# Kernel tuning notes

Measured on AMD Instinct MI355X. Metric: run time of the kernel, lower is better.

The kernel has to match this reference:

```python
import jax, jax.numpy as jnp
import numpy as np

B, S, D, H = 2, 2048, 1024, 16
DEPTH = D // H


def setup_inputs() -> dict:
    key = jax.random.key(0)
    ks = jax.random.split(key, 13)
    std = 1.0 / np.sqrt(D)
    inp = {
        'q': jax.random.normal(ks[0], (B, S, D), jnp.float32),
        'k': jax.random.normal(ks[1], (B, S, D), jnp.float32),
        'v': jax.random.normal(ks[2], (B, S, D), jnp.float32),
        # padding-style mask broadcastable to [B,H,Sq,Sk]; 1 = masked
        'mask': (jax.random.uniform(ks[3], (B, 1, 1, S)) < 0.1).astype(jnp.float32),
        'wq_w': jax.random.uniform(ks[4], (D, D), jnp.float32, -std, std),
        'wq_b': jax.random.uniform(ks[5], (D,), jnp.float32, -std, std),
        'wk_w': jax.random.uniform(ks[6], (D, D), jnp.float32, -std, std),
        'wk_b': jax.random.uniform(ks[7], (D,), jnp.float32, -std, std),
        'wv_w': jax.random.uniform(ks[8], (D, D), jnp.float32, -std, std),
        'wv_b': jax.random.uniform(ks[9], (D,), jnp.float32, -std, std),
        'wo_w': jax.random.uniform(ks[10], (D, D), jnp.float32, -std, std),
        'wo_b': jax.random.uniform(ks[11], (D,), jnp.float32, -std, std),
    }
    return inp


def _split_heads(x):
    # [B,S,D] -> [B,H,S,depth]
    b, s, _ = x.shape
    return x.reshape(b, s, H, DEPTH).transpose(0, 2, 1, 3)


def reference(q, k, v, mask, wq_w, wq_b, wk_w, wk_b, wv_w, wv_b, wo_w, wo_b):
    qh = _split_heads(q @ wq_w.T + wq_b)
    kh = _split_heads(k @ wk_w.T + wk_b)
    vh = _split_heads(v @ wv_w.T + wv_b)
    scale = 1.0 / jnp.sqrt(jnp.float32(DEPTH))
    logits = jnp.einsum('bhqd,bhkd->bhqk', qh, kh) * scale  # [B,H,S,S]
    logits = logits + mask * (-1e9)
    weights = jax.nn.softmax(logits, axis=-1)
    attn = jnp.einsum('bhqk,bhkd->bhqd', weights, vh)
    concat = attn.transpose(0, 2, 1, 3).reshape(q.shape[0], -1, D)
    out = concat @ wo_w.T + wo_b
    return out, weights
```

## Files before the change

### kernel.cpp

```cpp
#include <hip/hip_runtime.h>
#include <stdint.h>
#include <stddef.h>

static constexpr int NB = 2;
static constexpr int SS = 2048;
static constexpr int DDim = 1024;
static constexpr int NH = 16;
static constexpr size_t BSD = (size_t)NB * SS * DDim;
static constexpr size_t DDn = (size_t)DDim * DDim;

typedef __attribute__((ext_vector_type(4))) float f32x4;
typedef __attribute__((ext_vector_type(8))) short bf16x8;
typedef __attribute__((ext_vector_type(4))) short bf16x4;

static constexpr float SCL2 = 0.125f * 1.4426950408889634f;
static constexpr float MSK2 = -1.4426950408889634e9f;

__device__ __forceinline__ short f2bf(float f) {
  union { float f; unsigned u; } v; v.f = f;
  unsigned r = v.u + 0x7FFFu + ((v.u >> 16) & 1u);
  return (short)(r >> 16);
}

__device__ __forceinline__ void gload_lds16(const void* src, void* dst) {
  __builtin_amdgcn_global_load_lds(
      (const __attribute__((address_space(1))) void*)src,
      (__attribute__((address_space(3))) void*)dst, 16, 0, 0);
}

__global__ void cvt_all_k(const float* __restrict__ q, const float* __restrict__ k,
                          const float* __restrict__ v, const float* __restrict__ w0,
                          const float* __restrict__ w1, const float* __restrict__ w2,
                          const float* __restrict__ w3, short* __restrict__ out) {
  int i = blockIdx.x * 256 + threadIdx.x;
  const float* src;
  int j;
  if (i < 1572864) {
    int mat = i >> 19;
    src = mat == 0 ? q : mat == 1 ? k : v;
    j = i & 524287;
  } else {
    int t = i - 1572864;
    int mat = t >> 17;
    src = mat == 0 ? w0 : mat == 1 ? w1 : mat == 2 ? w2 : w3;
    j = t & 131071;
  }
  const f32x4* p = (const f32x4*)src + (size_t)j * 2;
  f32x4 a = p[0], c = p[1];
  bf16x8 o;
  o[0] = f2bf(a[0]); o[1] = f2bf(a[1]); o[2] = f2bf(a[2]); o[3] = f2bf(a[3]);
  o[4] = f2bf(c[0]); o[5] = f2bf(c[1]); o[6] = f2bf(c[2]); o[7] = f2bf(c[3]);
  ((bf16x8*)out)[i] = o;
}

__global__ __launch_bounds__(256, 2) void proj3_k(
    const short* __restrict__ Acat, const short* __restrict__ Bcat,
    const float* __restrict__ bq, const float* __restrict__ bk, const float* __restrict__ bv,
    short* __restrict__ qh, short* __restrict__ kh, short* __restrict__ vhT) {
  __shared__ short la[2][4096], lb[2][4096];
  const int tid = threadIdx.x, wid = tid >> 6, lane = tid & 63;
  const int proj = blockIdx.z;
  const short* A = Acat + (size_t)proj * BSD;
  const short* Bm = Bcat + (size_t)proj * DDn;
  const float* bias = proj == 0 ? bq : proj == 1 ? bk : bv;
  const int bM = blockIdx.y * 128, bN = blockIdx.x * 128;
  const int ar = lane & 15, ak = (lane >> 4) * 8;
  const int srow = lane >> 2, scol = (lane & 3) * 8;
  const int wr = wid >> 1, wc = wid & 1;
  f32x4 acc[4][4];
#pragma unroll
  for (int m = 0; m < 4; ++m)
#pragma unroll
    for (int n = 0; n < 4; ++n) acc[m][n] = (f32x4){0.f, 0.f, 0.f, 0.f};

  auto stage = [&](int kt, int bb) {
    const int k0 = kt * 32;
#pragma unroll
    for (int c = 0; c < 2; ++c) {
      int chunk = c * 4 + wid;
      gload_lds16(A + (size_t)(bM + chunk * 16 + srow) * DDim + k0 + scol, &la[bb][chunk * 512]);
      gload_lds16(Bm + (size_t)(bN + chunk * 16 + srow) * DDim + k0 + scol, &lb[bb][chunk * 512]);
    }
  };

  stage(0, 0);
  asm volatile("s_waitcnt vmcnt(0)" ::: "memory");
  __syncthreads();
  for (int kt = 0; kt < 32; ++kt) {
    const int bb = kt & 1;
    if (kt < 31) stage(kt + 1, bb ^ 1);
    bf16x8 af[4], bfr[4];
#pragma unroll
    for (int m = 0; m < 4; ++m)
      af[m] = *(const bf16x8*)(&la[bb][(wr * 64 + m * 16 + ar) * 32 + ak]);
#pragma unroll
    for (int n = 0; n < 4; ++n)
      bfr[n] = *(const bf16x8*)(&lb[bb][(wc * 64 + n * 16 + ar) * 32 + ak]);
#pragma unroll
    for (int m = 0; m < 4; ++m)
#pragma unroll
      for (int n = 0; n < 4; ++n)
        acc[m][n] = __builtin_amdgcn_mfma_f32_16x16x32_bf16(af[m], bfr[n], acc[m][n], 0, 0, 0);
    asm volatile("s_waitcnt vmcnt(0)" ::: "memory");
    __syncthreads();
  }
#pragma unroll
  for (int m = 0; m < 4; ++m)
#pragma unroll
    for (int n = 0; n < 4; ++n)
#pragma unroll
      for (int r = 0; r < 4; ++r) {
        int gm = bM + wr * 64 + m * 16 + (lane >> 4) * 4 + r;
        int gn = bN + wc * 64 + n * 16 + (lane & 15);
        float val = acc[m][n][r] + bias[gn];
        int b = gm >> 11, s = gm & 2047, h = gn >> 6, d = gn & 63;
        if (proj == 2)
          vhT[(((size_t)b * NH + h) * 64 + d) * SS + s] = f2bf(val);
        else {
          short* o = proj == 0 ? qh : kh;
          o[(((size_t)b * NH + h) * SS + s) * 64 + d] = f2bf(val);
        }
      }
}

__global__ __launch_bounds__(256, 2) void outproj_k(
    const short* __restrict__ A, const short* __restrict__ Bm,
    const float* __restrict__ bias, float* __restrict__ outp) {
  __shared__ short la[2][4096], lb[2][4096];
  const int tid = threadIdx.x, wid = tid >> 6, lane = tid & 63;
  const int bM = blockIdx.y * 128, bN = blockIdx.x * 128;
  const int ar = lane & 15, ak = (lane >> 4) * 8;
  const int srow = lane >> 2, scol = (lane & 3) * 8;
  const int wr = wid >> 1, wc = wid & 1;
  f32x4 acc[4][4];
#pragma unroll
  for (int m = 0; m < 4; ++m)
#pragma unroll
    for (int n = 0; n < 4; ++n) acc[m][n] = (f32x4){0.f, 0.f, 0.f, 0.f};

  auto stage = [&](int kt, int bb) {
    const int k0 = kt * 32;
#pragma unroll
    for (int c = 0; c < 2; ++c) {
      int chunk = c * 4 + wid;
      gload_lds16(A + (size_t)(bM + chunk * 16 + srow) * DDim + k0 + scol, &la[bb][chunk * 512]);
      gload_lds16(Bm + (size_t)(bN + chunk * 16 + srow) * DDim + k0 + scol, &lb[bb][chunk * 512]);
    }
  };

  stage(0, 0);
  asm volatile("s_waitcnt vmcnt(0)" ::: "memory");
  __syncthreads();
  for (int kt = 0; kt < 32; ++kt) {
    const int bb = kt & 1;
    if (kt < 31) stage(kt + 1, bb ^ 1);
    bf16x8 af[4], bfr[4];
#pragma unroll
    for (int m = 0; m < 4; ++m)
      af[m] = *(const bf16x8*)(&la[bb][(wr * 64 + m * 16 + ar) * 32 + ak]);
#pragma unroll
    for (int n = 0; n < 4; ++n)
      bfr[n] = *(const bf16x8*)(&lb[bb][(wc * 64 + n * 16 + ar) * 32 + ak]);
#pragma unroll
    for (int m = 0; m < 4; ++m)
#pragma unroll
      for (int n = 0; n < 4; ++n)
        acc[m][n] = __builtin_amdgcn_mfma_f32_16x16x32_bf16(af[m], bfr[n], acc[m][n], 0, 0, 0);
    asm volatile("s_waitcnt vmcnt(0)" ::: "memory");
    __syncthreads();
  }
#pragma unroll
  for (int m = 0; m < 4; ++m)
#pragma unroll
    for (int n = 0; n < 4; ++n)
#pragma unroll
      for (int r = 0; r < 4; ++r) {
        int gm = bM + wr * 64 + m * 16 + (lane >> 4) * 4 + r;
        int gn = bN + wc * 64 + n * 16 + (lane & 15);
        outp[(size_t)gm * DDim + gn] = acc[m][n][r] + bias[gn];
      }
}

__global__ __launch_bounds__(256, 2) void attn_k(
    const short* __restrict__ qh, const short* __restrict__ kh,
    const short* __restrict__ vhT, const float* __restrict__ mask,
    float* __restrict__ wout, short* __restrict__ concat) {
  __shared__ short lP[128 * 128];
  __shared__ short lK[128 * 64];
  __shared__ short lV[64 * 128];
  __shared__ float lmask[2048];
  __shared__ float lrs[2][128];
  const int tid = threadIdx.x, wid = tid >> 6, lane = tid & 63;
  const int wr = wid >> 1, wc = wid & 1;
  const int bh = blockIdx.y, b = bh >> 4, h = bh & 15;
  const int bM = blockIdx.x * 128;
  const short* Qb = qh + (size_t)bh * SS * 64 + (size_t)bM * 64;
  const short* Kb = kh + (size_t)bh * SS * 64;
  const short* Vb = vhT + (size_t)bh * 64 * SS;
  float* Wb = wout + (size_t)bh * SS * SS;

#pragma unroll
  for (int i = 0; i < 8; ++i)
    lmask[tid + i * 256] = mask[b * SS + tid + i * 256] * MSK2;

#pragma unroll
  for (int c = 0; c < 4; ++c) {
    int ob = c * 4096 + tid * 16;
    int row = ob >> 7, inrow = ob & 127;
    gload_lds16(Qb + row * 64 + ((inrow ^ ((row & 7) << 4)) >> 1), (char*)lP + ob);
  }
  asm volatile("s_waitcnt vmcnt(0)" ::: "memory");
  __syncthreads();
  bf16x8 af[4][2];
#pragma unroll
  for (int m = 0; m < 4; ++m)
#pragma unroll
    for (int kk = 0; kk < 2; ++kk) {
      int row = wr * 64 + m * 16 + (lane & 15);
      int kb = (kk * 32 + (lane >> 4) * 8) * 2;
      af[m][kk] = *(const bf16x8*)((const char*)lP + row * 128 + (kb ^ ((row & 7) << 4)));
    }

  float ps[4];
#pragma unroll
  for (int n = 0; n < 4; ++n) ps[n] = 0.f;

  for (int kt = 0; kt < 16; ++kt) {
    __syncthreads();
#pragma unroll
    for (int c = 0; c < 4; ++c) {
      int ob = c * 4096 + tid * 16;
      int row = ob >> 7, inrow = ob & 127;
      gload_lds16(Kb + (size_t)(kt * 128 + row) * 64 + ((inrow ^ ((row & 7) << 4)) >> 1),
                  (char*)lK + ob);
    }
    asm volatile("s_waitcnt vmcnt(0)" ::: "memory");
    __syncthreads();
    bf16x8 bfr[4][2];
#pragma unroll
    for (int mk = 0; mk < 4; ++mk)
#pragma unroll
      for (int kk = 0; kk < 2; ++kk) {
        int row = wc * 64 + mk * 16 + (lane & 15);
        int kb = (kk * 32 + (lane >> 4) * 8) * 2;
        bfr[mk][kk] = *(const bf16x8*)((const char*)lK + row * 128 + (kb ^ ((row & 7) << 4)));
      }
#pragma unroll
    for (int mk = 0; mk < 4; ++mk) {
      f32x4 mv4 = *(const f32x4*)&lmask[kt * 128 + wc * 64 + mk * 16 + (lane >> 4) * 4];
#pragma unroll
      for (int nq = 0; nq < 4; ++nq) {
        f32x4 a = (f32x4){0.f, 0.f, 0.f, 0.f};
        a = __builtin_amdgcn_mfma_f32_16x16x32_bf16(bfr[mk][0], af[nq][0], a, 0, 0, 0);
        a = __builtin_amdgcn_mfma_f32_16x16x32_bf16(bfr[mk][1], af[nq][1], a, 0, 0, 0);
#pragma unroll
        for (int r = 0; r < 4; ++r) ps[nq] += exp2f(a[r] * SCL2 + mv4[r]);
      }
    }
  }
#pragma unroll
  for (int n = 0; n < 4; ++n) {
    float s = ps[n];
    s += __shfl_xor(s, 16, 64);
    s += __shfl_xor(s, 32, 64);
    ps[n] = s;
  }
  if (lane < 16) {
#pragma unroll
    for (int n = 0; n < 4; ++n) lrs[wc][wr * 64 + n * 16 + lane] = ps[n];
  }
  __syncthreads();
  float inv[4];
#pragma unroll
  for (int n = 0; n < 4; ++n) {
    int row = wr * 64 + n * 16 + (lane & 15);
    inv[n] = 1.f / (lrs[0][row] + lrs[1][row]);
  }

  f32x4 pacc[4][2];
#pragma unroll
  for (int m = 0; m < 4; ++m)
#pragma unroll
    for (int n = 0; n < 2; ++n) pacc[m][n] = (f32x4){0.f, 0.f, 0.f, 0.f};

  for (int kt = 0; kt < 16; ++kt) {
    __syncthreads();
#pragma unroll
    for (int c = 0; c < 4; ++c) {
      int ob = c * 4096 + tid * 16;
      int row = ob >> 7, inrow = ob & 127;
      gload_lds16(Kb + (size_t)(kt * 128 + row) * 64 + ((inrow ^ ((row & 7) << 4)) >> 1),
                  (char*)lK + ob);
    }
#pragma unroll
    for (int c = 0; c < 4; ++c) {
      int ob = c * 4096 + tid * 16;
      int row = ob >> 8, inrow = ob & 255;
      gload_lds16(Vb + (size_t)row * SS + kt * 128 + ((inrow ^ ((row & 7) << 4)) >> 1),
                  (char*)lV + ob);
    }
    asm volatile("s_waitcnt vmcnt(0)" ::: "memory");
    __syncthreads();
    bf16x8 bfr[4][2];
#pragma unroll
    for (int mk = 0; mk < 4; ++mk)
#pragma unroll
      for (int kk = 0; kk < 2; ++kk) {
        int row = wc * 64 + mk * 16 + (lane & 15);
        int kb = (kk * 32 + (lane >> 4) * 8) * 2;
        bfr[mk][kk] = *(const bf16x8*)((const char*)lK + row * 128 + (kb ^ ((row & 7) << 4)));
      }
#pragma unroll
    for (int mk = 0; mk < 4; ++mk) {
      const int klocal = wc * 64 + mk * 16 + (lane >> 4) * 4;
      f32x4 mv4 = *(const f32x4*)&lmask[kt * 128 + klocal];
#pragma unroll
      for (int nq = 0; nq < 4; ++nq) {
        f32x4 a = (f32x4){0.f, 0.f, 0.f, 0.f};
        a = __builtin_amdgcn_mfma_f32_16x16x32_bf16(bfr[mk][0], af[nq][0], a, 0, 0, 0);
        a = __builtin_amdgcn_mfma_f32_16x16x32_bf16(bfr[mk][1], af[nq][1], a, 0, 0, 0);
        const int qrow = wr * 64 + nq * 16 + (lane & 15);
        f32x4 w4;
#pragma unroll
        for (int r = 0; r < 4; ++r) w4[r] = exp2f(a[r] * SCL2 + mv4[r]) * inv[nq];
        *(f32x4*)&Wb[(size_t)(bM + qrow) * SS + kt * 128 + klocal] = w4;
        bf16x4 p4;
        p4[0] = f2bf(w4[0]); p4[1] = f2bf(w4[1]); p4[2] = f2bf(w4[2]); p4[3] = f2bf(w4[3]);
        *(bf16x4*)((char*)lP + qrow * 256 + ((klocal * 2) ^ ((qrow & 7) << 4))) = p4;
      }
    }
    __syncthreads();
#pragma unroll
    for (int kk = 0; kk < 4; ++kk) {
      bf16x8 pa[4], bv[2];
      int kb = (kk * 32 + (lane >> 4) * 8) * 2;
#pragma unroll
      for (int m = 0; m < 4; ++m) {
        int row = wr * 64 + m * 16 + (lane & 15);
        pa[m] = *(const bf16x8*)((const char*)lP + row * 256 + (kb ^ ((row & 7) << 4)));
      }
#pragma unroll
      for (int n = 0; n < 2; ++n) {
        int d = wc * 32 + n * 16 + (lane & 15);
        bv[n] = *(const bf16x8*)((const char*)lV + d * 256 + (kb ^ ((d & 7) << 4)));
      }
#pragma unroll
      for (int m = 0; m < 4; ++m)
#pragma unroll
        for (int n = 0; n < 2; ++n)
          pacc[m][n] = __builtin_amdgcn_mfma_f32_16x16x32_bf16(pa[m], bv[n], pacc[m][n], 0, 0, 0);
    }
  }
#pragma unroll
  for (int m = 0; m < 4; ++m)
#pragma unroll
    for (int n = 0; n < 2; ++n)
#pragma unroll
      for (int r = 0; r < 4; ++r) {
        int s = bM + wr * 64 + m * 16 + (lane >> 4) * 4 + r;
        int d = wc * 32 + n * 16 + (lane & 15);
        concat[((size_t)(b * SS + s)) * DDim + h * 64 + d] = f2bf(pacc[m][n][r]);
      }
}

extern "C" void kernel_launch(void* const* d_in, const int* in_sizes, int n_in,
                              void* d_out, int out_size, void* d_ws, size_t ws_size,
                              hipStream_t stream) {
  const float* q = (const float*)d_in[0];
  const float* k = (const float*)d_in[1];
  const float* v = (const float*)d_in[2];
  const float* mask = (const float*)d_in[3];
  const float* wq_w = (const float*)d_in[4];
  const float* wq_b = (const float*)d_in[5];
  const float* wk_w = (const float*)d_in[6];
  const float* wk_b = (const float*)d_in[7];
  const float* wv_w = (const float*)d_in[8];
  const float* wv_b = (const float*)d_in[9];
  const float* wo_w = (const float*)d_in[10];
  const float* wo_b = (const float*)d_in[11];

  short* qb = (short*)d_ws;
  short* wqb = qb + 3 * BSD;
  short* wob = wqb + 3 * DDn;
  short* qh = wob + DDn;
  short* kh = qh + BSD;
  short* vhT = kh + BSD;
  short* concat = vhT + BSD;

  float* out0 = (float*)d_out;
  float* wts = out0 + BSD;

  cvt_all_k<<<8192, 256, 0, stream>>>(q, k, v, wq_w, wk_w, wv_w, wo_w, qb);

  dim3 gproj(DDim / 128, (NB * SS) / 128, 3);
  proj3_k<<<gproj, 256, 0, stream>>>(qb, wqb, wq_b, wk_b, wv_b, qh, kh, vhT);

  dim3 gattn(SS / 128, NB * NH);
  attn_k<<<gattn, 256, 0, stream>>>(qh, kh, vhT, mask, wts, concat);

  dim3 gout(DDim / 128, (NB * SS) / 128);
  outproj_k<<<gout, 256, 0, stream>>>(concat, wob, wo_b, out0);
}
```

Baseline: 317.1 us.

## Prefetch K/V tiles into registers to overlap global loads with attention compute

Replaces the synchronous global_load_lds staging of K and V tiles with register prefetch: the next tile is loaded into registers while the current tile is computed, then written to LDS behind lightweight lgkmcnt barriers. This is meant to hide global memory latency that previously stalled every iteration on vmcnt(0). The grid is also transposed so blocks of the same head are no longer adjacent in launch order, which changes cache locality for K/V. The cost is extra VGPR pressure under launch_bounds(256,2) and an additional barrier per iteration.

After: 361.9 us. +14.1%, slower.

```diff
diff --git a/kernel.cpp b/kernel.cpp
--- a/kernel.cpp
+++ b/kernel.cpp
@@ -26,6 +26,12 @@
   __builtin_amdgcn_global_load_lds(
       (const __attribute__((address_space(1))) void*)src,
       (__attribute__((address_space(3))) void*)dst, 16, 0, 0);
+}
+
+__device__ __forceinline__ void lds_barrier() {
+  asm volatile("s_waitcnt lgkmcnt(0)" ::: "memory");
+  __builtin_amdgcn_sched_barrier(0);
+  __builtin_amdgcn_s_barrier();
 }
 
 __global__ void cvt_all_k(const float* __restrict__ q, const float* __restrict__ k,
@@ -192,13 +198,41 @@
   __shared__ float lrs[2][128];
   const int tid = threadIdx.x, wid = tid >> 6, lane = tid & 63;
   const int wr = wid >> 1, wc = wid & 1;
-  const int bh = blockIdx.y, b = bh >> 4, h = bh & 15;
-  const int bM = blockIdx.x * 128;
+  const int bh = blockIdx.x, b = bh >> 4, h = bh & 15;
+  const int bM = blockIdx.y * 128;
   const short* Qb = qh + (size_t)bh * SS * 64 + (size_t)bM * 64;
   const short* Kb = kh + (size_t)bh * SS * 64;
   const short* Vb = vhT + (size_t)bh * 64 * SS;
   float* Wb = wout + (size_t)bh * SS * SS;
 
+  bf16x8 kreg[4], vreg[4];
+  auto ldK = [&](int kt) {
+#pragma unroll
+    for (int c = 0; c < 4; ++c) {
+      int ob = c * 4096 + tid * 16;
+      int row = ob >> 7, inrow = ob & 127;
+      kreg[c] = *(const bf16x8*)(Kb + (size_t)(kt * 128 + row) * 64 +
+                                 ((inrow ^ ((row & 7) << 4)) >> 1));
+    }
+  };
+  auto wrK = [&]() {
+#pragma unroll
+    for (int c = 0; c < 4; ++c) *(bf16x8*)((char*)lK + c * 4096 + tid * 16) = kreg[c];
+  };
+  auto ldV = [&](int kt) {
+#pragma unroll
+    for (int c = 0; c < 4; ++c) {
+      int ob = c * 4096 + tid * 16;
+      int row = ob >> 8, inrow = ob & 255;
+      vreg[c] = *(const bf16x8*)(Vb + (size_t)row * SS + kt * 128 +
+                                 ((inrow ^ ((row & 7) << 4)) >> 1));
+    }
+  };
+  auto wrV = [&]() {
+#pragma unroll
+    for (int c = 0; c < 4; ++c) *(bf16x8*)((char*)lV + c * 4096 + tid * 16) = vreg[c];
+  };
+
 #pragma unroll
   for (int i = 0; i < 8; ++i)
     lmask[tid + i * 256] = mask[b * SS + tid + i * 256] * MSK2;
@@ -209,7 +243,9 @@
     int row = ob >> 7, inrow = ob & 127;
     gload_lds16(Qb + row * 64 + ((inrow ^ ((row & 7) << 4)) >> 1), (char*)lP + ob);
   }
+  ldK(0);
   asm volatile("s_waitcnt vmcnt(0)" ::: "memory");
+  wrK();
   __syncthreads();
   bf16x8 af[4][2];
 #pragma unroll
@@ -226,16 +262,7 @@
   for (int n = 0; n < 4; ++n) ps[n] = 0.f;
 
   for (int kt = 0; kt < 16; ++kt) {
-    __syncthreads();
-#pragma unroll
-    for (int c = 0; c < 4; ++c) {
-      int ob = c * 4096 + tid * 16;
-      int row = ob >> 7, inrow = ob & 127;
-      gload_lds16(Kb + (size_t)(kt * 128 + row) * 64 + ((inrow ^ ((row & 7) << 4)) >> 1),
-                  (char*)lK + ob);
-    }
-    asm volatile("s_waitcnt vmcnt(0)" ::: "memory");
-    __syncthreads();
+    if (kt < 15) ldK(kt + 1);
     bf16x8 bfr[4][2];
 #pragma unroll
     for (int mk = 0; mk < 4; ++mk)
@@ -256,6 +283,11 @@
 #pragma unroll
         for (int r = 0; r < 4; ++r) ps[nq] += exp2f(a[r] * SCL2 + mv4[r]);
       }
+    }
+    lds_barrier();
+    if (kt < 15) {
+      wrK();
+      lds_barrier();
     }
   }
 #pragma unroll
@@ -269,6 +301,8 @@
 #pragma unroll
     for (int n = 0; n < 4; ++n) lrs[wc][wr * 64 + n * 16 + lane] = ps[n];
   }
+  ldK(0);
+  ldV(0);
   __syncthreads();
   float inv[4];
 #pragma unroll
@@ -276,6 +310,9 @@
     int row = wr * 64 + n * 16 + (lane & 15);
     inv[n] = 1.f / (lrs[0][row] + lrs[1][row]);
   }
+  wrK();
+  wrV();
+  __syncthreads();
 
   f32x4 pacc[4][2];
 #pragma unroll
@@ -284,23 +321,10 @@
     for (int n = 0; n < 2; ++n) pacc[m][n] = (f32x4){0.f, 0.f, 0.f, 0.f};
 
   for (int kt = 0; kt < 16; ++kt) {
-    __syncthreads();
-#pragma unroll
-    for (int c = 0; c < 4; ++c) {
-      int ob = c * 4096 + tid * 16;
-      int row = ob >> 7, inrow = ob & 127;
-      gload_lds16(Kb + (size_t)(kt * 128 + row) * 64 + ((inrow ^ ((row & 7) << 4)) >> 1),
-                  (char*)lK + ob);
-    }
-#pragma unroll
-    for (int c = 0; c < 4; ++c) {
-      int ob = c * 4096 + tid * 16;
-      int row = ob >> 8, inrow = ob & 255;
-      gload_lds16(Vb + (size_t)row * SS + kt * 128 + ((inrow ^ ((row & 7) << 4)) >> 1),
-                  (char*)lV + ob);
-    }
-    asm volatile("s_waitcnt vmcnt(0)" ::: "memory");
-    __syncthreads();
+    if (kt < 15) {
+      ldK(kt + 1);
+      ldV(kt + 1);
+    }
     bf16x8 bfr[4][2];
 #pragma unroll
     for (int mk = 0; mk < 4; ++mk)
@@ -329,7 +353,7 @@
         *(bf16x4*)((char*)lP + qrow * 256 + ((klocal * 2) ^ ((qrow & 7) << 4))) = p4;
       }
     }
-    __syncthreads();
+    lds_barrier();
 #pragma unroll
     for (int kk = 0; kk < 4; ++kk) {
       bf16x8 pa[4], bv[2];
@@ -349,6 +373,12 @@
 #pragma unroll
         for (int n = 0; n < 2; ++n)
           pacc[m][n] = __builtin_amdgcn_mfma_f32_16x16x32_bf16(pa[m], bv[n], pacc[m][n], 0, 0, 0);
+    }
+    lds_barrier();
+    if (kt < 15) {
+      wrK();
+      wrV();
+      lds_barrier();
     }
   }
 #pragma unroll
@@ -395,7 +425,7 @@
   dim3 gproj(DDim / 128, (NB * SS) / 128, 3);
   proj3_k<<<gproj, 256, 0, stream>>>(qb, wqb, wq_b, wk_b, wv_b, qh, kh, vhT);
 
-  dim3 gattn(SS / 128, NB * NH);
+  dim3 gattn(NB * NH, SS / 128);
   attn_k<<<gattn, 256, 0, stream>>>(qh, kh, vhT, mask, wts, concat);
 
   dim3 gout(DDim / 128, (NB * SS) / 128);
```

## Double-buffer K/V tiles in attention kernel with 64-wide key tiles

Applied to the files above, without the earlier changes.

The attention kernel now stages K and V through two LDS buffers with 64-key tiles instead of single 128-key tiles. The next tile's global-to-LDS loads are issued before computing on the current tile, so load latency overlaps with MFMA and exp work in both the row-sum pass and the weights/PV pass. The smaller tiles keep LDS usage about the same, but they double the iteration count and the number of barriers. The P buffer also shrinks to match the new tile width.

After: 351.6 us. 1.11x slower.

```diff
diff --git a/kernel.cpp b/kernel.cpp
--- a/kernel.cpp
+++ b/kernel.cpp
@@ -26,6 +26,12 @@
   __builtin_amdgcn_global_load_lds(
       (const __attribute__((address_space(1))) void*)src,
       (__attribute__((address_space(3))) void*)dst, 16, 0, 0);
+}
+
+__device__ __forceinline__ void lds_barrier() {
+  asm volatile("s_waitcnt lgkmcnt(0)" ::: "memory");
+  __builtin_amdgcn_sched_barrier(0);
+  __builtin_amdgcn_s_barrier();
 }
 
 __global__ void cvt_all_k(const float* __restrict__ q, const float* __restrict__ k,
@@ -185,9 +191,9 @@
     const short* __restrict__ qh, const short* __restrict__ kh,
     const short* __restrict__ vhT, const float* __restrict__ mask,
     float* __restrict__ wout, short* __restrict__ concat) {
-  __shared__ short lP[128 * 128];
-  __shared__ short lK[128 * 64];
-  __shared__ short lV[64 * 128];
+  __shared__ short lP[128 * 64];
+  __shared__ short lK[2][64 * 64];
+  __shared__ short lV[2][64 * 64];
   __shared__ float lmask[2048];
   __shared__ float lrs[2][128];
   const int tid = threadIdx.x, wid = tid >> 6, lane = tid & 63;
@@ -203,12 +209,32 @@
   for (int i = 0; i < 8; ++i)
     lmask[tid + i * 256] = mask[b * SS + tid + i * 256] * MSK2;
 
+  auto stageK = [&](int kt, int bb) {
+#pragma unroll
+    for (int c = 0; c < 2; ++c) {
+      int ob = c * 4096 + tid * 16;
+      int row = ob >> 7, inrow = ob & 127;
+      gload_lds16(Kb + (size_t)(kt * 64 + row) * 64 + ((inrow ^ ((row & 7) << 4)) >> 1),
+                  (char*)lK[bb] + ob);
+    }
+  };
+  auto stageV = [&](int kt, int bb) {
+#pragma unroll
+    for (int c = 0; c < 2; ++c) {
+      int ob = c * 4096 + tid * 16;
+      int row = ob >> 7, inrow = ob & 127;
+      gload_lds16(Vb + (size_t)row * SS + kt * 64 + ((inrow ^ ((row & 7) << 4)) >> 1),
+                  (char*)lV[bb] + ob);
+    }
+  };
+
 #pragma unroll
   for (int c = 0; c < 4; ++c) {
     int ob = c * 4096 + tid * 16;
     int row = ob >> 7, inrow = ob & 127;
     gload_lds16(Qb + row * 64 + ((inrow ^ ((row & 7) << 4)) >> 1), (char*)lP + ob);
   }
+  stageK(0, 0);
   asm volatile("s_waitcnt vmcnt(0)" ::: "memory");
   __syncthreads();
   bf16x8 af[4][2];
@@ -225,29 +251,21 @@
 #pragma unroll
   for (int n = 0; n < 4; ++n) ps[n] = 0.f;
 
-  for (int kt = 0; kt < 16; ++kt) {
-    __syncthreads();
-#pragma unroll
-    for (int c = 0; c < 4; ++c) {
-      int ob = c * 4096 + tid * 16;
-      int row = ob >> 7, inrow = ob & 127;
-      gload_lds16(Kb + (size_t)(kt * 128 + row) * 64 + ((inrow ^ ((row & 7) << 4)) >> 1),
-                  (char*)lK + ob);
-    }
-    asm volatile("s_waitcnt vmcnt(0)" ::: "memory");
-    __syncthreads();
-    bf16x8 bfr[4][2];
-#pragma unroll
-    for (int mk = 0; mk < 4; ++mk)
+  for (int kt = 0; kt < 32; ++kt) {
+    const int bb = kt & 1;
+    if (kt < 31) stageK(kt + 1, bb ^ 1);
+    bf16x8 bfr[2][2];
+#pragma unroll
+    for (int mk = 0; mk < 2; ++mk)
 #pragma unroll
       for (int kk = 0; kk < 2; ++kk) {
-        int row = wc * 64 + mk * 16 + (lane & 15);
+        int row = wc * 32 + mk * 16 + (lane & 15);
         int kb = (kk * 32 + (lane >> 4) * 8) * 2;
-        bfr[mk][kk] = *(const bf16x8*)((const char*)lK + row * 128 + (kb ^ ((row & 7) << 4)));
-      }
-#pragma unroll
-    for (int mk = 0; mk < 4; ++mk) {
-      f32x4 mv4 = *(const f32x4*)&lmask[kt * 128 + wc * 64 + mk * 16 + (lane >> 4) * 4];
+        bfr[mk][kk] = *(const bf16x8*)((const char*)lK[bb] + row * 128 + (kb ^ ((row & 7) << 4)));
+      }
+#pragma unroll
+    for (int mk = 0; mk < 2; ++mk) {
+      f32x4 mv4 = *(const f32x4*)&lmask[kt * 64 + wc * 32 + mk * 16 + (lane >> 4) * 4];
 #pragma unroll
       for (int nq = 0; nq < 4; ++nq) {
         f32x4 a = (f32x4){0.f, 0.f, 0.f, 0.f};
@@ -257,6 +275,8 @@
         for (int r = 0; r < 4; ++r) ps[nq] += exp2f(a[r] * SCL2 + mv4[r]);
       }
     }
+    asm volatile("s_waitcnt vmcnt(0)" ::: "memory");
+    __syncthreads();
   }
 #pragma unroll
   for (int n = 0; n < 4; ++n) {
@@ -269,6 +289,8 @@
 #pragma unroll
     for (int n = 0; n < 4; ++n) lrs[wc][wr * 64 + n * 16 + lane] = ps[n];
   }
+  stageK(0, 0);
+  stageV(0, 0);
   __syncthreads();
   float inv[4];
 #pragma unroll
@@ -276,6 +298,8 @@
     int row = wr * 64 + n * 16 + (lane & 15);
     inv[n] = 1.f / (lrs[0][row] + lrs[1][row]);
   }
+  asm volatile("s_waitcnt vmcnt(0)" ::: "memory");
+  __syncthreads();
 
   f32x4 pacc[4][2];
 #pragma unroll
@@ -283,37 +307,25 @@
 #pragma unroll
     for (int n = 0; n < 2; ++n) pacc[m][n] = (f32x4){0.f, 0.f, 0.f, 0.f};
 
-  for (int kt = 0; kt < 16; ++kt) {
-    __syncthreads();
-#pragma unroll
-    for (int c = 0; c < 4; ++c) {
-      int ob = c * 4096 + tid * 16;
-      int row = ob >> 7, inrow = ob & 127;
-      gload_lds16(Kb + (size_t)(kt * 128 + row) * 64 + ((inrow ^ ((row & 7) << 4)) >> 1),
-                  (char*)lK + ob);
-    }
-#pragma unroll
-    for (int c = 0; c < 4; ++c) {
-      int ob = c * 4096 + tid * 16;
-      int row = ob >> 8, inrow = ob & 255;
-      gload_lds16(Vb + (size_t)row * SS + kt * 128 + ((inrow ^ ((row & 7) << 4)) >> 1),
-                  (char*)lV + ob);
-    }
-    asm volatile("s_waitcnt vmcnt(0)" ::: "memory");
-    __syncthreads();
-    bf16x8 bfr[4][2];
-#pragma unroll
-    for (int mk = 0; mk < 4; ++mk)
+  for (int kt = 0; kt < 32; ++kt) {
+    const int bb = kt & 1;
+    if (kt < 31) {
+      stageK(kt + 1, bb ^ 1);
+      stageV(kt + 1, bb ^ 1);
+    }
+    bf16x8 bfr[2][2];
+#pragma unroll
+    for (int mk = 0; mk < 2; ++mk)
 #pragma unroll
       for (int kk = 0; kk < 2; ++kk) {
-        int row = wc * 64 + mk * 16 + (lane & 15);
+        int row = wc * 32 + mk * 16 + (lane & 15);
         int kb = (kk * 32 + (lane >> 4) * 8) * 2;
-        bfr[mk][kk] = *(const bf16x8*)((const char*)lK + row * 128 + (kb ^ ((row & 7) << 4)));
-      }
-#pragma unroll
-    for (int mk = 0; mk < 4; ++mk) {
-      const int klocal = wc * 64 + mk * 16 + (lane >> 4) * 4;
-      f32x4 mv4 = *(const f32x4*)&lmask[kt * 128 + klocal];
+        bfr[mk][kk] = *(const bf16x8*)((const char*)lK[bb] + row * 128 + (kb ^ ((row & 7) << 4)));
+      }
+#pragma unroll
+    for (int mk = 0; mk < 2; ++mk) {
+      const int klocal = wc * 32 + mk * 16 + (lane >> 4) * 4;
+      f32x4 mv4 = *(const f32x4*)&lmask[kt * 64 + klocal];
 #pragma unroll
       for (int nq = 0; nq < 4; ++nq) {
         f32x4 a = (f32x4){0.f, 0.f, 0.f, 0.f};
@@ -323,26 +335,27 @@
         f32x4 w4;
 #pragma unroll
         for (int r = 0; r < 4; ++r) w4[r] = exp2f(a[r] * SCL2 + mv4[r]) * inv[nq];
-        *(f32x4*)&Wb[(size_t)(bM + qrow) * SS + kt * 128 + klocal] = w4;
+        *(f32x4*)&Wb[(size_t)(bM + qrow) * SS + kt * 64 + klocal] = w4;
         bf16x4 p4;
         p4[0] = f2bf(w4[0]); p4[1] = f2bf(w4[1]); p4[2] = f2bf(w4[2]); p4[3] = f2bf(w4[3]);
-        *(bf16x4*)((char*)lP + qrow * 256 + ((klocal * 2) ^ ((qrow & 7) << 4))) = p4;
-      }
-    }
+        *(bf16x4*)((char*)lP + qrow * 128 + ((klocal * 2) ^ ((qrow & 7) << 4))) = p4;
+      }
+    }
+    asm volatile("s_waitcnt vmcnt(0)" ::: "memory");
     __syncthreads();
 #pragma unroll
-    for (int kk = 0; kk < 4; ++kk) {
+    for (int kk = 0; kk < 2; ++kk) {
       bf16x8 pa[4], bv[2];
       int kb = (kk * 32 + (lane >> 4) * 8) * 2;
 #pragma unroll
       for (int m = 0; m < 4; ++m) {
         int row = wr * 64 + m * 16 + (lane & 15);
-        pa[m] = *(const bf16x8*)((const char*)lP + row * 256 + (kb ^ ((row & 7) << 4)));
+        pa[m] = *(const bf16x8*)((const char*)lP + row * 128 + (kb ^ ((row & 7) << 4)));
       }
 #pragma unroll
       for (int n = 0; n < 2; ++n) {
         int d = wc * 32 + n * 16 + (lane & 15);
-        bv[n] = *(const bf16x8*)((const char*)lV + d * 256 + (kb ^ ((d & 7) << 4)));
+        bv[n] = *(const bf16x8*)((const char*)lV[bb] + d * 128 + (kb ^ ((d & 7) << 4)));
       }
 #pragma unroll
       for (int m = 0; m < 4; ++m)
@@ -350,6 +363,7 @@
         for (int n = 0; n < 2; ++n)
           pacc[m][n] = __builtin_amdgcn_mfma_f32_16x16x32_bf16(pa[m], bv[n], pacc[m][n], 0, 0, 0);
     }
+    lds_barrier();
   }
 #pragma unroll
   for (int m = 0; m < 4; ++m)
```

## Split attention into separate row-sum and PV kernels

Applied to the files above, without the earlier changes.

Moves the first pass (QK^T, exp, row-sum accumulation) out of the attention kernel into its own lighter kernel with smaller LDS footprint and higher launch-bounds occupancy, writing row sums to a workspace buffer. The PV kernel then reads the precomputed sums instead of recomputing them. This aims to raise occupancy for the sum pass, at the cost of an extra kernel launch and reloading Q/mask in the second kernel.

Result: slower. 340.5 us (+7.4%).

```diff
diff --git a/kernel.cpp b/kernel.cpp
--- a/kernel.cpp
+++ b/kernel.cpp
@@ -181,15 +181,109 @@
       }
 }
 
-__global__ __launch_bounds__(256, 2) void attn_k(
+__global__ __launch_bounds__(256, 3) void attn_sum_k(
+    const short* __restrict__ qh, const short* __restrict__ kh,
+    const float* __restrict__ mask, float* __restrict__ rowsum) {
+  __shared__ short lQ[128 * 64];
+  __shared__ short lK[128 * 64];
+  __shared__ float lmask[2048];
+  __shared__ float lrs[2][128];
+  const int tid = threadIdx.x, wid = tid >> 6, lane = tid & 63;
+  const int wr = wid >> 1, wc = wid & 1;
+  const int bh = blockIdx.y, b = bh >> 4;
+  const int bM = blockIdx.x * 128;
+  const short* Qb = qh + (size_t)bh * SS * 64 + (size_t)bM * 64;
+  const short* Kb = kh + (size_t)bh * SS * 64;
+
+#pragma unroll
+  for (int i = 0; i < 8; ++i)
+    lmask[tid + i * 256] = mask[b * SS + tid + i * 256] * MSK2;
+
+#pragma unroll
+  for (int c = 0; c < 4; ++c) {
+    int ob = c * 4096 + tid * 16;
+    int row = ob >> 7, inrow = ob & 127;
+    gload_lds16(Qb + row * 64 + ((inrow ^ ((row & 7) << 4)) >> 1), (char*)lQ + ob);
+  }
+  asm volatile("s_waitcnt vmcnt(0)" ::: "memory");
+  __syncthreads();
+  bf16x8 af[4][2];
+#pragma unroll
+  for (int m = 0; m < 4; ++m)
+#pragma unroll
+    for (int kk = 0; kk < 2; ++kk) {
+      int row = wr * 64 + m * 16 + (lane & 15);
+      int kb = (kk * 32 + (lane >> 4) * 8) * 2;
+      af[m][kk] = *(const bf16x8*)((const char*)lQ + row * 128 + (kb ^ ((row & 7) << 4)));
+    }
+
+  float ps[4];
+#pragma unroll
+  for (int n = 0; n < 4; ++n) ps[n] = 0.f;
+
+  for (int kt = 0; kt < 16; ++kt) {
+    __syncthreads();
+#pragma unroll
+    for (int c = 0; c < 4; ++c) {
+      int ob = c * 4096 + tid * 16;
+      int row = ob >> 7, inrow = ob & 127;
+      gload_lds16(Kb + (size_t)(kt * 128 + row) * 64 + ((inrow ^ ((row & 7) << 4)) >> 1),
+                  (char*)lK + ob);
+    }
+    asm volatile("s_waitcnt vmcnt(0)" ::: "memory");
+    __syncthreads();
+    bf16x8 bfr[4][2];
+#pragma unroll
+    for (int mk = 0; mk < 4; ++mk)
+#pragma unroll
+      for (int kk = 0; kk < 2; ++kk) {
+        int row = wc * 64 + mk * 16 + (lane & 15);
+        int kb = (kk * 32 + (lane >> 4) * 8) * 2;
+        bfr[mk][kk] = *(const bf16x8*)((const char*)lK + row * 128 + (kb ^ ((row & 7) << 4)));
+      }
+#pragma unroll
+    for (int mk = 0; mk < 4; ++mk) {
+      f32x4 mv4 = *(const f32x4*)&lmask[kt * 128 + wc * 64 + mk * 16 + (lane >> 4) * 4];
+#pragma unroll
+      for (int nq = 0; nq < 4; ++nq) {
+        f32x4 a = (f32x4){0.f, 0.f, 0.f, 0.f};
+        a = __builtin_amdgcn_mfma_f32_16x16x32_bf16(bfr[mk][0], af[nq][0], a, 0, 0, 0);
+        a = __builtin_amdgcn_mfma_f32_16x16x32_bf16(bfr[mk][1], af[nq][1], a, 0, 0, 0);
+#pragma unroll
+        for (int r = 0; r < 4; ++r) ps[nq] += exp2f(a[r] * SCL2 + mv4[r]);
+      }
+    }
+  }
+#pragma unroll
+  for (int n = 0; n < 4; ++n) {
+    float s = ps[n];
+    s += __shfl_xor(s, 16, 64);
+    s += __shfl_xor(s, 32, 64);
+    ps[n] = s;
+  }
+  if (lane < 16) {
+#pragma unroll
+    for (int n = 0; n < 4; ++n) lrs[wc][wr * 64 + n * 16 + lane] = ps[n];
+  }
+  __syncthreads();
+  if (wc == 0 && lane < 16) {
+#pragma unroll
+    for (int n = 0; n < 4; ++n) {
+      int row = wr * 64 + n * 16 + lane;
+      rowsum[(size_t)bh * SS + bM + row] = lrs[0][row] + lrs[1][row];
+    }
+  }
+}
+
+__global__ __launch_bounds__(256, 2) void attn_pv_k(
     const short* __restrict__ qh, const short* __restrict__ kh,
     const short* __restrict__ vhT, const float* __restrict__ mask,
-    float* __restrict__ wout, short* __restrict__ concat) {
+    const float* __restrict__ rowsum, float* __restrict__ wout,
+    short* __restrict__ concat) {
   __shared__ short lP[128 * 128];
   __shared__ short lK[128 * 64];
   __shared__ short lV[64 * 128];
   __shared__ float lmask[2048];
-  __shared__ float lrs[2][128];
   const int tid = threadIdx.x, wid = tid >> 6, lane = tid & 63;
   const int wr = wid >> 1, wc = wid & 1;
   const int bh = blockIdx.y, b = bh >> 4, h = bh & 15;
@@ -220,61 +314,11 @@
       int kb = (kk * 32 + (lane >> 4) * 8) * 2;
       af[m][kk] = *(const bf16x8*)((const char*)lP + row * 128 + (kb ^ ((row & 7) << 4)));
     }
-
-  float ps[4];
-#pragma unroll
-  for (int n = 0; n < 4; ++n) ps[n] = 0.f;
-
-  for (int kt = 0; kt < 16; ++kt) {
-    __syncthreads();
-#pragma unroll
-    for (int c = 0; c < 4; ++c) {
-      int ob = c * 4096 + tid * 16;
-      int row = ob >> 7, inrow = ob & 127;
-      gload_lds16(Kb + (size_t)(kt * 128 + row) * 64 + ((inrow ^ ((row & 7) << 4)) >> 1),
-                  (char*)lK + ob);
-    }
-    asm volatile("s_waitcnt vmcnt(0)" ::: "memory");
-    __syncthreads();
-    bf16x8 bfr[4][2];
-#pragma unroll
-    for (int mk = 0; mk < 4; ++mk)
-#pragma unroll
-      for (int kk = 0; kk < 2; ++kk) {
-        int row = wc * 64 + mk * 16 + (lane & 15);
-        int kb = (kk * 32 + (lane >> 4) * 8) * 2;
-        bfr[mk][kk] = *(const bf16x8*)((const char*)lK + row * 128 + (kb ^ ((row & 7) << 4)));
-      }
-#pragma unroll
-    for (int mk = 0; mk < 4; ++mk) {
-      f32x4 mv4 = *(const f32x4*)&lmask[kt * 128 + wc * 64 + mk * 16 + (lane >> 4) * 4];
-#pragma unroll
-      for (int nq = 0; nq < 4; ++nq) {
-        f32x4 a = (f32x4){0.f, 0.f, 0.f, 0.f};
-        a = __builtin_amdgcn_mfma_f32_16x16x32_bf16(bfr[mk][0], af[nq][0], a, 0, 0, 0);
-        a = __builtin_amdgcn_mfma_f32_16x16x32_bf16(bfr[mk][1], af[nq][1], a, 0, 0, 0);
-#pragma unroll
-        for (int r = 0; r < 4; ++r) ps[nq] += exp2f(a[r] * SCL2 + mv4[r]);
-      }
-    }
-  }
-#pragma unroll
-  for (int n = 0; n < 4; ++n) {
-    float s = ps[n];
-    s += __shfl_xor(s, 16, 64);
-    s += __shfl_xor(s, 32, 64);
-    ps[n] = s;
-  }
-  if (lane < 16) {
-#pragma unroll
-    for (int n = 0; n < 4; ++n) lrs[wc][wr * 64 + n * 16 + lane] = ps[n];
-  }
-  __syncthreads();
   float inv[4];
 #pragma unroll
   for (int n = 0; n < 4; ++n) {
     int row = wr * 64 + n * 16 + (lane & 15);
-    inv[n] = 1.f / (lrs[0][row] + lrs[1][row]);
+    inv[n] = 1.f / rowsum[(size_t)bh * SS + bM + row];
   }
 
   f32x4 pacc[4][2];
@@ -386,6 +430,7 @@
   short* kh = qh + BSD;
   short* vhT = kh + BSD;
   short* concat = vhT + BSD;
+  float* rowsum = (float*)(concat + BSD);
 
   float* out0 = (float*)d_out;
   float* wts = out0 + BSD;
@@ -396,7 +441,8 @@
   proj3_k<<<gproj, 256, 0, stream>>>(qb, wqb, wq_b, wk_b, wv_b, qh, kh, vhT);
 
   dim3 gattn(SS / 128, NB * NH);
-  attn_k<<<gattn, 256, 0, stream>>>(qh, kh, vhT, mask, wts, concat);
+  attn_sum_k<<<gattn, 256, 0, stream>>>(qh, kh, mask, rowsum);
+  attn_pv_k<<<gattn, 256, 0, stream>>>(qh, kh, vhT, mask, rowsum, wts, concat);
 
   dim3 gout(DDim / 128, (NB * SS) / 128);
   outproj_k<<<gout, 256, 0, stream>>>(concat, wob, wo_b, out0);
```
